# Optimization experiments

Measured on AMD Instinct MI355X. Metric: run time of the kernel, lower is better.

## Reference

```python
import math
import jax, jax.numpy as jnp
import numpy as np

B, S, D, H, FF, E, V, RH = 8, 256, 512, 8, 2048, 8, 32000, 256
MAX_PATH, MAX_VISITS = 4, 2
NEG = -1e9
DH = D // H


def _make_pe():
    # PositionalEncoding buffer (sin/cos), sliced to seq len S
    pos = np.arange(S, dtype=np.float32)[:, None]
    div = np.exp(np.arange(0, D, 2, dtype=np.float32) * (-math.log(10000.0) / D))
    pe = np.zeros((S, D), dtype=np.float32)
    pe[:, 0::2] = np.sin(pos * div)
    pe[:, 1::2] = np.cos(pos * div)
    return jnp.asarray(pe[None])  # [1,S,D]


def setup_inputs() -> dict:
    key = jax.random.key(0)
    ks = jax.random.split(key, 12)
    s = 0.02
    return dict(
        input_ids=jax.random.randint(ks[0], (B, S), 0, V),
        emb=jax.random.normal(ks[1], (V, D), jnp.float32) * s,
        pe=_make_pe(),
        Wqkv=jax.random.normal(ks[2], (E, 3 * D, D), jnp.float32) * s,
        bqkv=jnp.zeros((E, 3 * D), jnp.float32),
        Wo=jax.random.normal(ks[3], (E, D, D), jnp.float32) * s,
        bo=jnp.zeros((E, D), jnp.float32),
        W1=jax.random.normal(ks[4], (E, FF, D), jnp.float32) * s,
        b1=jnp.zeros((E, FF), jnp.float32),
        W2=jax.random.normal(ks[5], (E, D, FF), jnp.float32) * s,
        b2=jnp.zeros((E, D), jnp.float32),
        ln1_g=jnp.ones((E, D), jnp.float32), ln1_b=jnp.zeros((E, D), jnp.float32),
        ln2_g=jnp.ones((E, D), jnp.float32), ln2_b=jnp.zeros((E, D), jnp.float32),
        tag=jax.random.normal(ks[6], (E, D), jnp.float32) * 0.01,
        r_w1=jax.random.normal(ks[7], (RH, D), jnp.float32) * s,
        r_b1=jnp.zeros((RH,), jnp.float32),
        r_w2=jax.random.normal(ks[8], (E + 1, RH), jnp.float32) * s,
        r_b2=jnp.zeros((E + 1,), jnp.float32),
        lm_w=jax.random.normal(ks[9], (V, D), jnp.float32) * s,
        lm_b=jnp.zeros((V,), jnp.float32),
    )


def _ln(x, g, b):
    # per-sample gathered LayerNorm params g,b: [B,D]; x: [B,S,D]
    mu = x.mean(-1, keepdims=True)
    var = ((x - mu) ** 2).mean(-1, keepdims=True)
    return (x - mu) * jax.lax.rsqrt(var + 1e-5) * g[:, None, :] + b[:, None, :]


def _expert(x, idx, Wqkv, bqkv, Wo, bo, W1, b1, W2, b2, g1, be1, g2, be2, tag):
    # post-norm TransformerEncoderLayer (eval mode, dropout off) with per-sample expert params
    qkv = jnp.einsum('bsd,bfd->bsf', x, Wqkv[idx]) + bqkv[idx][:, None, :]
    q, k, v = jnp.split(qkv, 3, axis=-1)
    q = q.reshape(B, S, H, DH)
    k = k.reshape(B, S, H, DH)
    v = v.reshape(B, S, H, DH)
    att = jax.nn.softmax(jnp.einsum('bqhd,bkhd->bhqk', q, k) / math.sqrt(DH), axis=-1)
    ctx = jnp.einsum('bhqk,bkhd->bqhd', att, v).reshape(B, S, D)
    attn_out = jnp.einsum('bsd,bod->bso', ctx, Wo[idx]) + bo[idx][:, None, :]
    x = _ln(x + attn_out, g1[idx], be1[idx])
    hid = jax.nn.relu(jnp.einsum('bsd,bfd->bsf', x, W1[idx]) + b1[idx][:, None, :])
    ff = jnp.einsum('bsf,bdf->bsd', hid, W2[idx]) + b2[idx][:, None, :]
    x = _ln(x + ff, g2[idx], be2[idx])
    return x + tag[idx][:, None, :]  # + specialization_tag


def reference(input_ids, emb, pe, Wqkv, bqkv, Wo, bo, W1, b1, W2, b2,
              ln1_g, ln1_b, ln2_g, ln2_b, tag, r_w1, r_b1, r_w2, r_b2, lm_w, lm_b):
    pad_mask = (jnp.arange(V) != 0).astype(emb.dtype)[:, None]  # padding_idx=0 row is zero
    rep = (emb * pad_mask)[input_ids] * math.sqrt(D) + pe[:, :S]
    visits = jnp.zeros((B, E), jnp.int32)
    active = jnp.ones((B,), bool)
    ent_total = jnp.asarray(0.0, rep.dtype)
    for _ in range(MAX_PATH):
        summary = rep.mean(1)  # [B,D]
        h = jax.nn.relu(summary @ r_w1.T + r_b1)
        logits = h @ r_w2.T + r_b2  # [B,E+1], last slot = terminate
        logits = jnp.concatenate(
            [jnp.where(visits >= MAX_VISITS, NEG, logits[:, :E]), logits[:, E:]], axis=1)
        probs = jax.nn.softmax(logits, axis=-1)
        ent = -jnp.sum(probs * jnp.log(probs + 1e-9), axis=-1)
        cnt = jnp.sum(active)
        ent_total = ent_total + jnp.where(
            cnt > 0, jnp.sum(ent * active) / jnp.maximum(cnt, 1).astype(ent.dtype), 0.0)
        choice = jnp.argmax(logits, axis=-1)       # eval mode: hard argmax
        go = active & (choice < E)                 # samples routed to an expert this step
        idx = jnp.where(go, choice, 0)
        visits = visits + jax.nn.one_hot(idx, E, dtype=jnp.int32) * go[:, None].astype(jnp.int32)
        new_rep = _expert(rep, idx, Wqkv, bqkv, Wo, bo, W1, b1, W2, b2,
                          ln1_g, ln1_b, ln2_g, ln2_b, tag)
        rep = jnp.where(go[:, None, None], new_rep, rep)  # terminated/inactive reps frozen
        active = go
    logits_lm = rep @ lm_w.T + lm_b  # [B,S,V]
    return logits_lm, ent_total
```

## Files before the change

kernel.cpp:

```cpp
#include <hip/hip_runtime.h>
#include <hip/hip_bf16.h>

#define NB 8
#define NS 256
#define ND 512
#define NH 8
#define NDH 64
#define NFF 2048
#define NE 8
#define NV 32000
#define NRH 256
#define MAXV 2
#define NEGV (-1e9f)

typedef __attribute__((ext_vector_type(8))) short short8;
typedef __attribute__((ext_vector_type(4))) float f32x4;

__device__ __forceinline__ unsigned short f2bf(float x) {
  unsigned int u = __float_as_uint(x);
  u = (u + 0x7fffu + ((u >> 16) & 1u)) >> 16;
  return (unsigned short)u;
}

__device__ __forceinline__ void gload16(const unsigned short* g, unsigned short* l) {
  __builtin_amdgcn_global_load_lds(
      (const __attribute__((address_space(1))) unsigned int*)g,
      (__attribute__((address_space(3))) unsigned int*)l, 16, 0, 0);
}

__device__ __forceinline__ int swzc(int lane) {
  return (lane & 3) ^ ((lane >> 3) & 3);
}

__device__ __forceinline__ void cast8(const float* s, unsigned short* d, int j) {
  const float4* s4 = (const float4*)s;
  float4 a = s4[j * 2], b = s4[j * 2 + 1];
  short8 v;
  v[0] = (short)f2bf(a.x); v[1] = (short)f2bf(a.y);
  v[2] = (short)f2bf(a.z); v[3] = (short)f2bf(a.w);
  v[4] = (short)f2bf(b.x); v[5] = (short)f2bf(b.y);
  v[6] = (short)f2bf(b.z); v[7] = (short)f2bf(b.w);
  *(short8*)&d[(size_t)j * 8] = v;
}

__global__ __launch_bounds__(256) void k_cast5(
    const float* s0, unsigned short* d0, int n0,
    const float* s1, unsigned short* d1, int n1,
    const float* s2, unsigned short* d2, int n2,
    const float* s3, unsigned short* d3, int n3,
    const float* s4, unsigned short* d4, int n4,
    int* visits, int* active, float* entp) {
  if (blockIdx.x == 0) {
    if (threadIdx.x < NB * NE) visits[threadIdx.x] = 0;
    if (threadIdx.x < NB) active[threadIdx.x] = 1;
    if (threadIdx.x == 0) *entp = 0.f;
  }
  int j = blockIdx.x * 256 + threadIdx.x;
  if (j < n0) { cast8(s0, d0, j); return; }
  j -= n0;
  if (j < n1) { cast8(s1, d1, j); return; }
  j -= n1;
  if (j < n2) { cast8(s2, d2, j); return; }
  j -= n2;
  if (j < n3) { cast8(s3, d3, j); return; }
  j -= n3;
  if (j < n4) cast8(s4, d4, j);
}

__global__ __launch_bounds__(256) void k_embed16(const int* __restrict__ ids,
                                                 const float* __restrict__ emb,
                                                 const float* __restrict__ pe,
                                                 float* __restrict__ rep,
                                                 unsigned short* __restrict__ repb,
                                                 float* __restrict__ partial) {
  int rg = blockIdx.x, b = blockIdx.y;
  int t = threadIdx.x;
  int c0 = t, c1 = t + 256;
  float p0 = 0.f, p1 = 0.f;
  for (int row = 0; row < 16; ++row) {
    int s = rg * 16 + row;
    int id = ids[b * NS + s];
    float sc = (id != 0) ? 22.627416997969522f : 0.f;
    float v0 = emb[(size_t)id * ND + c0] * sc + pe[(size_t)s * ND + c0];
    float v1 = emb[(size_t)id * ND + c1] * sc + pe[(size_t)s * ND + c1];
    size_t base = ((size_t)b * NS + s) * ND;
    rep[base + c0] = v0; rep[base + c1] = v1;
    repb[base + c0] = f2bf(v0); repb[base + c1] = f2bf(v1);
    p0 += v0; p1 += v1;
  }
  float* pp = partial + ((size_t)b * 16 + rg) * ND;
  pp[c0] = p0; pp[c1] = p1;
}

__global__ __launch_bounds__(256) void k_router(const float* __restrict__ partial,
                                                const float* __restrict__ rw1,
                                                const float* __restrict__ rb1,
                                                const float* __restrict__ rw2,
                                                const float* __restrict__ rb2,
                                                int* visits, int* active,
                                                int* idx, int* go, float* ent_total) {
  __shared__ float sm[NB][ND];
  __shared__ float h[NB][NRH];
  __shared__ float lg[NB][NE + 1];
  int t = threadIdx.x;
  for (int i = t; i < NB * ND; i += 256) {
    int bb = i >> 9, d = i & 511;
    const float* pp = partial + ((size_t)bb * 16) * ND + d;
    float s = 0.f;
#pragma unroll
    for (int rg = 0; rg < 16; ++rg) s += pp[(size_t)rg * ND];
    sm[bb][d] = s * (1.f / NS);
  }
  __syncthreads();
  {
    const float* w = rw1 + (size_t)t * ND;
    float acc[NB];
#pragma unroll
    for (int b = 0; b < NB; ++b) acc[b] = rb1[t];
    for (int d = 0; d < ND; ++d) {
      float wv = w[d];
#pragma unroll
      for (int b = 0; b < NB; ++b) acc[b] += sm[b][d] * wv;
    }
#pragma unroll
    for (int b = 0; b < NB; ++b) h[b][t] = fmaxf(acc[b], 0.f);
  }
  __syncthreads();
  if (t < NB * (NE + 1)) {
    int b = t / (NE + 1), e = t % (NE + 1);
    const float* w = rw2 + e * NRH;
    float a = rb2[e];
    for (int r = 0; r < NRH; ++r) a += h[b][r] * w[r];
    lg[b][e] = a;
  }
  __syncthreads();
  if (t == 0) {
    int aprev[NB];
    int cnt = 0;
    for (int b = 0; b < NB; ++b) { aprev[b] = active[b]; cnt += aprev[b]; }
    float entsum = 0.f;
    for (int b = 0; b < NB; ++b) {
      float l[NE + 1];
      for (int e = 0; e < NE; ++e)
        l[e] = (visits[b * NE + e] >= MAXV) ? NEGV : lg[b][e];
      l[NE] = lg[b][NE];
      float m = l[0];
      for (int e = 1; e <= NE; ++e) m = fmaxf(m, l[e]);
      float z = 0.f, p[NE + 1];
      for (int e = 0; e <= NE; ++e) { p[e] = __expf(l[e] - m); z += p[e]; }
      float zi = 1.f / z, ent = 0.f;
      for (int e = 0; e <= NE; ++e) {
        float pp = p[e] * zi;
        ent -= pp * __logf(pp + 1e-9f);
      }
      if (aprev[b]) entsum += ent;
      int ch = 0; float bm = l[0];
      for (int e = 1; e <= NE; ++e) if (l[e] > bm) { bm = l[e]; ch = e; }
      int g = (aprev[b] && ch < NE) ? 1 : 0;
      int ix = g ? ch : 0;
      visits[b * NE + ix] += g;
      idx[b] = ix; go[b] = g; active[b] = g;
    }
    if (cnt > 0) *ent_total += entsum / (float)cnt;
  }
}

template <int OUT, int RELU>
__global__ __launch_bounds__(256) void k_gemm64(
    const unsigned short* __restrict__ Aall, int sa,
    const unsigned short* __restrict__ Wall, const float* __restrict__ ball,
    float* __restrict__ Fall, unsigned short* __restrict__ Uall, int so,
    int N, int K,
    unsigned short* __restrict__ Qb, unsigned short* __restrict__ Kb,
    unsigned short* __restrict__ Vt,
    const int* __restrict__ go, const int* __restrict__ idx) {
  int b = blockIdx.z;
  if (!go[b]) return;
  int t = threadIdx.x;
  int lane = t & 63, w = t >> 6;
  int wm = (w >> 1) * 32, wn = (w & 1) * 32;
  int bm = blockIdx.x * 64, bn = blockIdx.y * 64;
  int lrow = (lane >> 4) * 4, lcol = lane & 15;
  const unsigned short* A = Aall + (size_t)b * sa;
  const unsigned short* W = Wall + (size_t)idx[b] * N * K;
  const float* bias = ball + (size_t)idx[b] * N;

  __shared__ __align__(16) unsigned short As[2][64][32];
  __shared__ __align__(16) unsigned short Bs[2][64][32];
  f32x4 acc[2][2];
#pragma unroll
  for (int i = 0; i < 2; ++i)
#pragma unroll
    for (int j = 0; j < 2; ++j) acc[i][j] = (f32x4){0.f, 0.f, 0.f, 0.f};

  const unsigned short* ga = A + (size_t)(bm + w * 16 + (lane >> 2)) * K + swzc(lane) * 8;
  const unsigned short* gb = W + (size_t)(bn + w * 16 + (lane >> 2)) * K + swzc(lane) * 8;

  gload16(ga, &As[0][w * 16][0]);
  gload16(gb, &Bs[0][w * 16][0]);
  __syncthreads();

  int nk = K >> 5;
  int row0 = lane & 15;
  int cs = ((lane >> 4) ^ ((row0 >> 1) & 3)) * 8;
  for (int it = 0; it < nk; ++it) {
    int cur = it & 1;
    if (it + 1 < nk) {
      gload16(ga + (it + 1) * 32, &As[cur ^ 1][w * 16][0]);
      gload16(gb + (it + 1) * 32, &Bs[cur ^ 1][w * 16][0]);
    }
    short8 a[2], bfr[2];
#pragma unroll
    for (int mf = 0; mf < 2; ++mf)
      a[mf] = *(const short8*)&As[cur][wm + mf * 16 + row0][cs];
#pragma unroll
    for (int nf = 0; nf < 2; ++nf)
      bfr[nf] = *(const short8*)&Bs[cur][wn + nf * 16 + row0][cs];
#pragma unroll
    for (int mf = 0; mf < 2; ++mf)
#pragma unroll
      for (int nf = 0; nf < 2; ++nf)
        acc[mf][nf] = __builtin_amdgcn_mfma_f32_16x16x32_bf16(a[mf], bfr[nf], acc[mf][nf], 0, 0, 0);
    __syncthreads();
  }

  if (OUT == 2) {
    int seg = bn >> 9;
#pragma unroll
    for (int nf = 0; nf < 2; ++nf) {
      int col = bn + wn + nf * 16 + lcol;
      float bv = bias[col];
      if (seg < 2) {
        unsigned short* dst = (seg == 0) ? Qb : Kb;
        int cc = col - seg * 512;
#pragma unroll
        for (int mf = 0; mf < 2; ++mf)
#pragma unroll
          for (int r = 0; r < 4; ++r) {
            int row = bm + wm + mf * 16 + lrow + r;
            dst[((size_t)b * NS + row) * ND + cc] = f2bf(acc[mf][nf][r] + bv);
          }
      } else {
        int dcol = col - 1024;
#pragma unroll
        for (int mf = 0; mf < 2; ++mf) {
          int s0 = bm + wm + mf * 16 + lrow;
          unsigned long long pk =
              (unsigned long long)f2bf(acc[mf][nf][0] + bv) |
              ((unsigned long long)f2bf(acc[mf][nf][1] + bv) << 16) |
              ((unsigned long long)f2bf(acc[mf][nf][2] + bv) << 32) |
              ((unsigned long long)f2bf(acc[mf][nf][3] + bv) << 48);
          *(unsigned long long*)&Vt[((size_t)b * 512 + dcol) * 256 + s0] = pk;
        }
      }
    }
  } else {
#pragma unroll
    for (int nf = 0; nf < 2; ++nf) {
      int col = bn + wn + nf * 16 + lcol;
      float bv = bias[col];
#pragma unroll
      for (int mf = 0; mf < 2; ++mf) {
#pragma unroll
        for (int r = 0; r < 4; ++r) {
          int row = bm + wm + mf * 16 + lrow + r;
          float v = acc[mf][nf][r] + bv;
          if (RELU) v = fmaxf(v, 0.f);
          if (OUT == 0)
            Fall[(size_t)b * so + (size_t)row * N + col] = v;
          else
            Uall[(size_t)b * so + (size_t)row * N + col] = f2bf(v);
        }
      }
    }
  }
}

__global__ __launch_bounds__(256) void k_attn2(const unsigned short* __restrict__ Qb,
                                               const unsigned short* __restrict__ Kb,
                                               const unsigned short* __restrict__ Vt,
                                               unsigned short* __restrict__ ctxb,
                                               const int* __restrict__ go) {
  int b = blockIdx.z, h = blockIdx.y, qt = blockIdx.x;
  if (!go[b]) return;
  int t = threadIdx.x;
  __shared__ __align__(16) unsigned short lds0[16384];
  __shared__ __align__(16) unsigned short lds1[16384];
  int lane = t & 63, w = t >> 6, g = lane >> 4, c = lane & 15;

#pragma unroll
  for (int i = 0; i < 8; ++i) {
    int task = i * 256 + t;
    int k = task >> 3, cc = task & 7;
    short8 v = *(const short8*)&Kb[((size_t)b * NS + k) * ND + h * NDH + cc * 8];
    *(short8*)&lds0[k * 64 + ((cc * 8) ^ ((k & 7) << 3))] = v;
  }
#pragma unroll
  for (int i = 0; i < 8; ++i) {
    int task = i * 256 + t;
    int d = task >> 5, kc = task & 31;
    short8 v = *(const short8*)&Vt[((size_t)b * 512 + h * NDH + d) * 256 + kc * 8];
    *(short8*)&lds1[d * 256 + ((kc * 8) ^ ((d & 7) << 3))] = v;
  }
  short8 qf[2];
  {
    const unsigned short* qp = Qb + ((size_t)b * NS + qt * 64 + w * 16 + c) * ND + h * NDH;
    qf[0] = *(const short8*)&qp[g * 8];
    qf[1] = *(const short8*)&qp[32 + g * 8];
  }
  __syncthreads();

  f32x4 sacc[16];
#pragma unroll
  for (int mf = 0; mf < 16; ++mf) sacc[mf] = (f32x4){0.f, 0.f, 0.f, 0.f};
#pragma unroll
  for (int mf = 0; mf < 16; ++mf) {
#pragma unroll
    for (int kd = 0; kd < 2; ++kd) {
      int row = mf * 16 + c;
      short8 kf = *(const short8*)&lds0[row * 64 + ((kd * 32 + g * 8) ^ ((row & 7) << 3))];
      sacc[mf] = __builtin_amdgcn_mfma_f32_16x16x32_bf16(kf, qf[kd], sacc[mf], 0, 0, 0);
    }
  }
  __syncthreads();

  float mx = -3.4e38f;
#pragma unroll
  for (int mf = 0; mf < 16; ++mf) {
#pragma unroll
    for (int r = 0; r < 4; ++r) {
      sacc[mf][r] *= 0.125f;
      mx = fmaxf(mx, sacc[mf][r]);
    }
  }
  mx = fmaxf(mx, __shfl_xor(mx, 16));
  mx = fmaxf(mx, __shfl_xor(mx, 32));
  float sum = 0.f;
#pragma unroll
  for (int mf = 0; mf < 16; ++mf)
#pragma unroll
    for (int r = 0; r < 4; ++r) {
      float p = __expf(sacc[mf][r] - mx);
      sacc[mf][r] = p;
      sum += p;
    }
  sum += __shfl_xor(sum, 16);
  sum += __shfl_xor(sum, 32);
  float zi = 1.f / sum;

  int q_l = w * 16 + c;
#pragma unroll
  for (int mf = 0; mf < 16; ++mf) {
    unsigned long long pk =
        (unsigned long long)f2bf(sacc[mf][0] * zi) |
        ((unsigned long long)f2bf(sacc[mf][1] * zi) << 16) |
        ((unsigned long long)f2bf(sacc[mf][2] * zi) << 32) |
        ((unsigned long long)f2bf(sacc[mf][3] * zi) << 48);
    *(unsigned long long*)&lds0[q_l * 256 + ((mf * 16 + g * 4) ^ ((q_l & 7) << 3))] = pk;
  }

  f32x4 cacc[4];
#pragma unroll
  for (int nf = 0; nf < 4; ++nf) cacc[nf] = (f32x4){0.f, 0.f, 0.f, 0.f};
#pragma unroll
  for (int ks = 0; ks < 8; ++ks) {
    int prow = w * 16 + c;
    short8 pf = *(const short8*)&lds0[prow * 256 + ((ks * 32 + g * 8) ^ ((prow & 7) << 3))];
#pragma unroll
    for (int nf = 0; nf < 4; ++nf) {
      int vrow = nf * 16 + c;
      short8 vf = *(const short8*)&lds1[vrow * 256 + ((ks * 32 + g * 8) ^ ((vrow & 7) << 3))];
      cacc[nf] = __builtin_amdgcn_mfma_f32_16x16x32_bf16(pf, vf, cacc[nf], 0, 0, 0);
    }
  }
#pragma unroll
  for (int nf = 0; nf < 4; ++nf)
#pragma unroll
    for (int r = 0; r < 4; ++r)
      ctxb[((size_t)b * NS + qt * 64 + w * 16 + g * 4 + r) * ND + h * NDH + nf * 16 + c] =
          f2bf(cacc[nf][r]);
}

__global__ __launch_bounds__(256) void k_lnw(const float* __restrict__ xin,
                                             const float* __restrict__ yin,
                                             const float* __restrict__ gall,
                                             const float* __restrict__ ball,
                                             float* __restrict__ outf,
                                             unsigned short* __restrict__ outb,
                                             const int* __restrict__ go,
                                             const int* __restrict__ idx) {
  int b = blockIdx.y;
  if (!go[b]) return;
  int w = threadIdx.x >> 6, l = threadIdx.x & 63;
  int s = blockIdx.x * 4 + w;
  size_t base = ((size_t)b * NS + s) * ND;
  int d = l * 8;
  float4 x0 = *(const float4*)&xin[base + d];
  float4 x1 = *(const float4*)&xin[base + d + 4];
  float4 y0 = *(const float4*)&yin[base + d];
  float4 y1 = *(const float4*)&yin[base + d + 4];
  float v[8] = {x0.x + y0.x, x0.y + y0.y, x0.z + y0.z, x0.w + y0.w,
                x1.x + y1.x, x1.y + y1.y, x1.z + y1.z, x1.w + y1.w};
  float sum = 0.f;
#pragma unroll
  for (int j = 0; j < 8; ++j) sum += v[j];
#pragma unroll
  for (int off = 1; off < 64; off <<= 1) sum += __shfl_xor(sum, off);
  float mu = sum * (1.f / ND);
  float var = 0.f;
#pragma unroll
  for (int j = 0; j < 8; ++j) { v[j] -= mu; var += v[j] * v[j]; }
#pragma unroll
  for (int off = 1; off < 64; off <<= 1) var += __shfl_xor(var, off);
  float rs = rsqrtf(var * (1.f / ND) + 1e-5f);
  int ix = idx[b];
  float4 g0 = *(const float4*)&gall[ix * ND + d];
  float4 g1 = *(const float4*)&gall[ix * ND + d + 4];
  float4 b0 = *(const float4*)&ball[ix * ND + d];
  float4 b1 = *(const float4*)&ball[ix * ND + d + 4];
  float gg[8] = {g0.x, g0.y, g0.z, g0.w, g1.x, g1.y, g1.z, g1.w};
  float bb[8] = {b0.x, b0.y, b0.z, b0.w, b1.x, b1.y, b1.z, b1.w};
  float o[8];
#pragma unroll
  for (int j = 0; j < 8; ++j) o[j] = v[j] * rs * gg[j] + bb[j];
  *(float4*)&outf[base + d] = (float4){o[0], o[1], o[2], o[3]};
  *(float4*)&outf[base + d + 4] = (float4){o[4], o[5], o[6], o[7]};
  short8 ob;
#pragma unroll
  for (int j = 0; j < 8; ++j) ob[j] = (short)f2bf(o[j]);
  *(short8*)&outb[base + d] = ob;
}

__global__ __launch_bounds__(256) void k_lnw_p(const float* __restrict__ xin,
                                               const float* __restrict__ yin,
                                               const float* __restrict__ gall,
                                               const float* __restrict__ ball,
                                               const float* __restrict__ tagall,
                                               float* __restrict__ outf,
                                               unsigned short* __restrict__ outb,
                                               float* __restrict__ partial,
                                               const int* __restrict__ go,
                                               const int* __restrict__ idx) {
  int b = blockIdx.y;
  if (!go[b]) return;
  int rg = blockIdx.x;
  int w = threadIdx.x >> 6, l = threadIdx.x & 63;
  int ix = idx[b];
  int d = l * 8;
  float4 g0 = *(const float4*)&gall[ix * ND + d];
  float4 g1 = *(const float4*)&gall[ix * ND + d + 4];
  float4 b0 = *(const float4*)&ball[ix * ND + d];
  float4 b1 = *(const float4*)&ball[ix * ND + d + 4];
  float4 t0 = *(const float4*)&tagall[ix * ND + d];
  float4 t1 = *(const float4*)&tagall[ix * ND + d + 4];
  float gg[8] = {g0.x, g0.y, g0.z, g0.w, g1.x, g1.y, g1.z, g1.w};
  float bb[8] = {b0.x + t0.x, b0.y + t0.y, b0.z + t0.z, b0.w + t0.w,
                 b1.x + t1.x, b1.y + t1.y, b1.z + t1.z, b1.w + t1.w};
  float p[8] = {0.f, 0.f, 0.f, 0.f, 0.f, 0.f, 0.f, 0.f};
  for (int rr = 0; rr < 4; ++rr) {
    int s = rg * 16 + w * 4 + rr;
    size_t base = ((size_t)b * NS + s) * ND;
    float4 x0 = *(const float4*)&xin[base + d];
    float4 x1 = *(const float4*)&xin[base + d + 4];
    float4 y0 = *(const float4*)&yin[base + d];
    float4 y1 = *(const float4*)&yin[base + d + 4];
    float v[8] = {x0.x + y0.x, x0.y + y0.y, x0.z + y0.z, x0.w + y0.w,
                  x1.x + y1.x, x1.y + y1.y, x1.z + y1.z, x1.w + y1.w};
    float sum = 0.f;
#pragma unroll
    for (int j = 0; j < 8; ++j) sum += v[j];
#pragma unroll
    for (int off = 1; off < 64; off <<= 1) sum += __shfl_xor(sum, off);
    float mu = sum * (1.f / ND);
    float var = 0.f;
#pragma unroll
    for (int j = 0; j < 8; ++j) { v[j] -= mu; var += v[j] * v[j]; }
#pragma unroll
    for (int off = 1; off < 64; off <<= 1) var += __shfl_xor(var, off);
    float rs = rsqrtf(var * (1.f / ND) + 1e-5f);
    float o[8];
    short8 ob;
#pragma unroll
    for (int j = 0; j < 8; ++j) {
      o[j] = v[j] * rs * gg[j] + bb[j];
      p[j] += o[j];
      ob[j] = (short)f2bf(o[j]);
    }
    *(float4*)&outf[base + d] = (float4){o[0], o[1], o[2], o[3]};
    *(float4*)&outf[base + d + 4] = (float4){o[4], o[5], o[6], o[7]};
    *(short8*)&outb[base + d] = ob;
  }
  __shared__ float pl[4][ND];
#pragma unroll
  for (int j = 0; j < 8; ++j) pl[w][d + j] = p[j];
  __syncthreads();
  if (w == 0) {
    float* pp = partial + ((size_t)b * 16 + rg) * ND;
#pragma unroll
    for (int j = 0; j < 8; ++j)
      pp[d + j] = pl[0][d + j] + pl[1][d + j] + pl[2][d + j] + pl[3][d + j];
  }
}

__global__ __launch_bounds__(512, 2) void k_lmhead256(const unsigned short* __restrict__ Ab,
                                                      const unsigned short* __restrict__ Wb,
                                                      const float* __restrict__ bias,
                                                      float* __restrict__ out,
                                                      const float* __restrict__ entp) {
  if (blockIdx.x == 0 && threadIdx.x == 0)
    out[(size_t)NB * NS * NV] = *entp;
  int id = blockIdx.x;
  int swz = (id & 7) * 125 + (id >> 3);
  int bm = (swz % 8) * 256;
  int bn = (swz / 8) * 256;

  __shared__ __align__(16) unsigned short As[2][256][32];
  __shared__ __align__(16) unsigned short Bs[2][256][32];
  int t = threadIdx.x;
  int lane = t & 63, w = t >> 6;
  int wm = (w >> 2) * 128, wn = (w & 3) * 64;
  f32x4 acc[8][4];
#pragma unroll
  for (int i = 0; i < 8; ++i)
#pragma unroll
    for (int j = 0; j < 4; ++j) acc[i][j] = (f32x4){0.f, 0.f, 0.f, 0.f};

  const unsigned short* ga = Ab + (size_t)(bm + w * 32 + (lane >> 2)) * ND + swzc(lane) * 8;
  const unsigned short* gb = Wb + (size_t)(bn + w * 32 + (lane >> 2)) * ND + swzc(lane) * 8;

  gload16(ga, &As[0][w * 32][0]);
  gload16(ga + 16 * ND, &As[0][w * 32 + 16][0]);
  gload16(gb, &Bs[0][w * 32][0]);
  gload16(gb + 16 * ND, &Bs[0][w * 32 + 16][0]);
  __syncthreads();

  int row0 = lane & 15;
  int cs = ((lane >> 4) ^ ((row0 >> 1) & 3)) * 8;
  for (int it = 0; it < 16; ++it) {
    int cur = it & 1;
    if (it < 15) {
      int k0 = (it + 1) * 32;
      gload16(ga + k0, &As[cur ^ 1][w * 32][0]);
      gload16(ga + k0 + 16 * ND, &As[cur ^ 1][w * 32 + 16][0]);
      gload16(gb + k0, &Bs[cur ^ 1][w * 32][0]);
      gload16(gb + k0 + 16 * ND, &Bs[cur ^ 1][w * 32 + 16][0]);
    }
    short8 a[8], bfr[4];
#pragma unroll
    for (int mf = 0; mf < 8; ++mf)
      a[mf] = *(const short8*)&As[cur][wm + mf * 16 + row0][cs];
#pragma unroll
    for (int nf = 0; nf < 4; ++nf)
      bfr[nf] = *(const short8*)&Bs[cur][wn + nf * 16 + row0][cs];
#pragma unroll
    for (int mf = 0; mf < 8; ++mf)
#pragma unroll
      for (int nf = 0; nf < 4; ++nf)
        acc[mf][nf] = __builtin_amdgcn_mfma_f32_16x16x32_bf16(a[mf], bfr[nf], acc[mf][nf], 0, 0, 0);
    __syncthreads();
  }
  int lrow = (lane >> 4) * 4, lcol = lane & 15;
#pragma unroll
  for (int nf = 0; nf < 4; ++nf) {
    int col = bn + wn + nf * 16 + lcol;
    float bv = bias[col];
#pragma unroll
    for (int mf = 0; mf < 8; ++mf) {
#pragma unroll
      for (int r = 0; r < 4; ++r) {
        int row = bm + wm + mf * 16 + lrow + r;
        out[(size_t)row * NV + col] = acc[mf][nf][r] + bv;
      }
    }
  }
}

extern "C" void kernel_launch(void* const* d_in, const int* in_sizes, int n_in,
                              void* d_out, int out_size, void* d_ws, size_t ws_size,
                              hipStream_t stream) {
  const int* ids   = (const int*)d_in[0];
  const float* emb = (const float*)d_in[1];
  const float* pe  = (const float*)d_in[2];
  const float* Wqkv = (const float*)d_in[3];
  const float* bqkv = (const float*)d_in[4];
  const float* Wo   = (const float*)d_in[5];
  const float* bo   = (const float*)d_in[6];
  const float* W1   = (const float*)d_in[7];
  const float* b1   = (const float*)d_in[8];
  const float* W2   = (const float*)d_in[9];
  const float* b2   = (const float*)d_in[10];
  const float* g1   = (const float*)d_in[11];
  const float* be1  = (const float*)d_in[12];
  const float* g2   = (const float*)d_in[13];
  const float* be2  = (const float*)d_in[14];
  const float* tag  = (const float*)d_in[15];
  const float* rw1  = (const float*)d_in[16];
  const float* rb1  = (const float*)d_in[17];
  const float* rw2  = (const float*)d_in[18];
  const float* rb2  = (const float*)d_in[19];
  const float* lmw  = (const float*)d_in[20];
  const float* lmb  = (const float*)d_in[21];
  float* out = (float*)d_out;

  float* ws = (float*)d_ws;
  size_t o = 0;
  float* rep = ws + o;  o += (size_t)NB * NS * ND;
  float* x1  = ws + o;  o += (size_t)NB * NS * ND;
  float* tmp = ws + o;  o += (size_t)NB * NS * ND;
  float* partial = ws + o; o += (size_t)NB * 16 * ND;
  int* visits = (int*)(ws + o); o += 1024;
  int* active = visits + NB * NE;
  int* idx = active + NB;
  int* go = idx + NB;
  float* entp = (float*)(go + NB);

  unsigned short* us = (unsigned short*)(ws + o);
  size_t uo = 0;
  unsigned short* rep_b = us + uo; uo += (size_t)NB * NS * ND;
  unsigned short* x1_b  = us + uo; uo += (size_t)NB * NS * ND;
  unsigned short* ctx_b = us + uo; uo += (size_t)NB * NS * ND;
  unsigned short* Qb    = us + uo; uo += (size_t)NB * NS * ND;
  unsigned short* Kb    = us + uo; uo += (size_t)NB * NS * ND;
  unsigned short* Vt    = us + uo; uo += (size_t)NB * NS * ND;
  unsigned short* hid_b = us + uo; uo += (size_t)NB * NS * NFF;
  unsigned short* Wqkv_b = us + uo; uo += (size_t)NE * 3 * ND * ND;
  unsigned short* Wo_b   = us + uo; uo += (size_t)NE * ND * ND;
  unsigned short* W1_b   = us + uo; uo += (size_t)NE * NFF * ND;
  unsigned short* W2_b   = us + uo; uo += (size_t)NE * ND * NFF;
  unsigned short* lmw_b  = us + uo; uo += (size_t)NV * ND;

  {
    int n0 = NE * 3 * ND * ND / 8, n1 = NE * ND * ND / 8, n2 = NE * NFF * ND / 8,
        n3 = NE * ND * NFF / 8, n4 = NV * ND / 8;
    int nblk = (n0 + n1 + n2 + n3 + n4) / 256;
    k_cast5<<<nblk, 256, 0, stream>>>(Wqkv, Wqkv_b, n0, Wo, Wo_b, n1,
                                      W1, W1_b, n2, W2, W2_b, n3, lmw, lmw_b, n4,
                                      visits, active, entp);
  }

  k_embed16<<<dim3(16, NB), 256, 0, stream>>>(ids, emb, pe, rep, rep_b, partial);

  for (int step = 0; step < 4; ++step) {
    k_router<<<1, 256, 0, stream>>>(partial, rw1, rb1, rw2, rb2,
                                    visits, active, idx, go, entp);
    k_gemm64<2, 0><<<dim3(4, 24, NB), 256, 0, stream>>>(
        rep_b, NS * ND, Wqkv_b, bqkv, nullptr, nullptr, 0, 3 * ND, ND,
        Qb, Kb, Vt, go, idx);
    k_attn2<<<dim3(4, NH, NB), 256, 0, stream>>>(Qb, Kb, Vt, ctx_b, go);
    k_gemm64<0, 0><<<dim3(4, 8, NB), 256, 0, stream>>>(
        ctx_b, NS * ND, Wo_b, bo, tmp, nullptr, NS * ND, ND, ND,
        nullptr, nullptr, nullptr, go, idx);
    k_lnw<<<dim3(NS / 4, NB), 256, 0, stream>>>(rep, tmp, g1, be1,
                                                x1, x1_b, go, idx);
    k_gemm64<1, 1><<<dim3(4, 32, NB), 256, 0, stream>>>(
        x1_b, NS * ND, W1_b, b1, nullptr, hid_b, NS * NFF, NFF, ND,
        nullptr, nullptr, nullptr, go, idx);
    k_gemm64<0, 0><<<dim3(4, 8, NB), 256, 0, stream>>>(
        hid_b, NS * NFF, W2_b, b2, tmp, nullptr, NS * ND, ND, NFF,
        nullptr, nullptr, nullptr, go, idx);
    k_lnw_p<<<dim3(16, NB), 256, 0, stream>>>(x1, tmp, g2, be2, tag,
                                              rep, rep_b, partial, go, idx);
  }

  k_lmhead256<<<1000, 512, 0, stream>>>(rep_b, lmw_b, lmb, out, entp);
}
```

Before: 626.6 us.

## Split-K the narrow GEMMs, widen N tiles, fold embed into the cast kernel

The Wo and W2 projections (N=512) now use split-K across 2 and 4 chunks, writing fp32 partials. The following LayerNorm kernel sums those partials and adds the bias, which raises parallelism on the low-block-count GEMMs. The QKV and W1 GEMMs switch to 64x128 tiles so more B data is reused per block. The embedding kernel is merged into the weight-cast launch to save one launch. The cost is extra partial-buffer traffic (up to 4 fp32 copies of the activations) and more registers per thread in the wider tiles.

```diff
diff --git a/kernel.cpp b/kernel.cpp
--- a/kernel.cpp
+++ b/kernel.cpp
@@ -43,17 +43,42 @@
   *(short8*)&d[(size_t)j * 8] = v;
 }
 
-__global__ __launch_bounds__(256) void k_cast5(
+__global__ __launch_bounds__(256) void k_cast5e(
     const float* s0, unsigned short* d0, int n0,
     const float* s1, unsigned short* d1, int n1,
     const float* s2, unsigned short* d2, int n2,
     const float* s3, unsigned short* d3, int n3,
     const float* s4, unsigned short* d4, int n4,
+    int nbcast,
+    const int* __restrict__ ids, const float* __restrict__ emb,
+    const float* __restrict__ pe, float* __restrict__ rep,
+    unsigned short* __restrict__ repb, float* __restrict__ partial,
     int* visits, int* active, float* entp) {
   if (blockIdx.x == 0) {
     if (threadIdx.x < NB * NE) visits[threadIdx.x] = 0;
     if (threadIdx.x < NB) active[threadIdx.x] = 1;
     if (threadIdx.x == 0) *entp = 0.f;
+  }
+  if ((int)blockIdx.x >= nbcast) {
+    int j2 = blockIdx.x - nbcast;
+    int rg = j2 & 15, b = j2 >> 4;
+    int t = threadIdx.x;
+    int c0 = t, c1 = t + 256;
+    float p0 = 0.f, p1 = 0.f;
+    for (int row = 0; row < 16; ++row) {
+      int s = rg * 16 + row;
+      int id = ids[b * NS + s];
+      float sc = (id != 0) ? 22.627416997969522f : 0.f;
+      float v0 = emb[(size_t)id * ND + c0] * sc + pe[(size_t)s * ND + c0];
+      float v1 = emb[(size_t)id * ND + c1] * sc + pe[(size_t)s * ND + c1];
+      size_t base = ((size_t)b * NS + s) * ND;
+      rep[base + c0] = v0; rep[base + c1] = v1;
+      repb[base + c0] = f2bf(v0); repb[base + c1] = f2bf(v1);
+      p0 += v0; p1 += v1;
+    }
+    float* pp = partial + ((size_t)b * 16 + rg) * ND;
+    pp[c0] = p0; pp[c1] = p1;
+    return;
   }
   int j = blockIdx.x * 256 + threadIdx.x;
   if (j < n0) { cast8(s0, d0, j); return; }
@@ -65,31 +90,6 @@
   if (j < n3) { cast8(s3, d3, j); return; }
   j -= n3;
   if (j < n4) cast8(s4, d4, j);
-}
-
-__global__ __launch_bounds__(256) void k_embed16(const int* __restrict__ ids,
-                                                 const float* __restrict__ emb,
-                                                 const float* __restrict__ pe,
-                                                 float* __restrict__ rep,
-                                                 unsigned short* __restrict__ repb,
-                                                 float* __restrict__ partial) {
-  int rg = blockIdx.x, b = blockIdx.y;
-  int t = threadIdx.x;
-  int c0 = t, c1 = t + 256;
-  float p0 = 0.f, p1 = 0.f;
-  for (int row = 0; row < 16; ++row) {
-    int s = rg * 16 + row;
-    int id = ids[b * NS + s];
-    float sc = (id != 0) ? 22.627416997969522f : 0.f;
-    float v0 = emb[(size_t)id * ND + c0] * sc + pe[(size_t)s * ND + c0];
-    float v1 = emb[(size_t)id * ND + c1] * sc + pe[(size_t)s * ND + c1];
-    size_t base = ((size_t)b * NS + s) * ND;
-    rep[base + c0] = v0; rep[base + c1] = v1;
-    repb[base + c0] = f2bf(v0); repb[base + c1] = f2bf(v1);
-    p0 += v0; p1 += v1;
-  }
-  float* pp = partial + ((size_t)b * 16 + rg) * ND;
-  pp[c0] = p0; pp[c1] = p1;
 }
 
 __global__ __launch_bounds__(256) void k_router(const float* __restrict__ partial,
@@ -166,11 +166,10 @@
 }
 
 template <int OUT, int RELU>
-__global__ __launch_bounds__(256) void k_gemm64(
+__global__ __launch_bounds__(256) void k_gemmN128(
     const unsigned short* __restrict__ Aall, int sa,
     const unsigned short* __restrict__ Wall, const float* __restrict__ ball,
-    float* __restrict__ Fall, unsigned short* __restrict__ Uall, int so,
-    int N, int K,
+    unsigned short* __restrict__ Uall, int so, int N, int K,
     unsigned short* __restrict__ Qb, unsigned short* __restrict__ Kb,
     unsigned short* __restrict__ Vt,
     const int* __restrict__ go, const int* __restrict__ idx) {
@@ -178,26 +177,27 @@
   if (!go[b]) return;
   int t = threadIdx.x;
   int lane = t & 63, w = t >> 6;
-  int wm = (w >> 1) * 32, wn = (w & 1) * 32;
-  int bm = blockIdx.x * 64, bn = blockIdx.y * 64;
+  int wm = (w >> 1) * 32, wn = (w & 1) * 64;
+  int bm = blockIdx.x * 64, bn = blockIdx.y * 128;
   int lrow = (lane >> 4) * 4, lcol = lane & 15;
   const unsigned short* A = Aall + (size_t)b * sa;
   const unsigned short* W = Wall + (size_t)idx[b] * N * K;
   const float* bias = ball + (size_t)idx[b] * N;
 
   __shared__ __align__(16) unsigned short As[2][64][32];
-  __shared__ __align__(16) unsigned short Bs[2][64][32];
-  f32x4 acc[2][2];
+  __shared__ __align__(16) unsigned short Bs[2][128][32];
+  f32x4 acc[2][4];
 #pragma unroll
   for (int i = 0; i < 2; ++i)
 #pragma unroll
-    for (int j = 0; j < 2; ++j) acc[i][j] = (f32x4){0.f, 0.f, 0.f, 0.f};
+    for (int j = 0; j < 4; ++j) acc[i][j] = (f32x4){0.f, 0.f, 0.f, 0.f};
 
   const unsigned short* ga = A + (size_t)(bm + w * 16 + (lane >> 2)) * K + swzc(lane) * 8;
-  const unsigned short* gb = W + (size_t)(bn + w * 16 + (lane >> 2)) * K + swzc(lane) * 8;
+  const unsigned short* gb = W + (size_t)(bn + w * 32 + (lane >> 2)) * K + swzc(lane) * 8;
 
   gload16(ga, &As[0][w * 16][0]);
-  gload16(gb, &Bs[0][w * 16][0]);
+  gload16(gb, &Bs[0][w * 32][0]);
+  gload16(gb + 16 * (size_t)K, &Bs[0][w * 32 + 16][0]);
   __syncthreads();
 
   int nk = K >> 5;
@@ -207,19 +207,20 @@
     int cur = it & 1;
     if (it + 1 < nk) {
       gload16(ga + (it + 1) * 32, &As[cur ^ 1][w * 16][0]);
-      gload16(gb + (it + 1) * 32, &Bs[cur ^ 1][w * 16][0]);
-    }
-    short8 a[2], bfr[2];
+      gload16(gb + (it + 1) * 32, &Bs[cur ^ 1][w * 32][0]);
+      gload16(gb + (it + 1) * 32 + 16 * (size_t)K, &Bs[cur ^ 1][w * 32 + 16][0]);
+    }
+    short8 a[2], bfr[4];
 #pragma unroll
     for (int mf = 0; mf < 2; ++mf)
       a[mf] = *(const short8*)&As[cur][wm + mf * 16 + row0][cs];
 #pragma unroll
-    for (int nf = 0; nf < 2; ++nf)
+    for (int nf = 0; nf < 4; ++nf)
       bfr[nf] = *(const short8*)&Bs[cur][wn + nf * 16 + row0][cs];
 #pragma unroll
     for (int mf = 0; mf < 2; ++mf)
 #pragma unroll
-      for (int nf = 0; nf < 2; ++nf)
+      for (int nf = 0; nf < 4; ++nf)
         acc[mf][nf] = __builtin_amdgcn_mfma_f32_16x16x32_bf16(a[mf], bfr[nf], acc[mf][nf], 0, 0, 0);
     __syncthreads();
   }
@@ -227,7 +228,7 @@
   if (OUT == 2) {
     int seg = bn >> 9;
 #pragma unroll
-    for (int nf = 0; nf < 2; ++nf) {
+    for (int nf = 0; nf < 4; ++nf) {
       int col = bn + wn + nf * 16 + lcol;
       float bv = bias[col];
       if (seg < 2) {
@@ -256,7 +257,7 @@
     }
   } else {
 #pragma unroll
-    for (int nf = 0; nf < 2; ++nf) {
+    for (int nf = 0; nf < 4; ++nf) {
       int col = bn + wn + nf * 16 + lcol;
       float bv = bias[col];
 #pragma unroll
@@ -266,13 +267,79 @@
           int row = bm + wm + mf * 16 + lrow + r;
           float v = acc[mf][nf][r] + bv;
           if (RELU) v = fmaxf(v, 0.f);
-          if (OUT == 0)
-            Fall[(size_t)b * so + (size_t)row * N + col] = v;
-          else
-            Uall[(size_t)b * so + (size_t)row * N + col] = f2bf(v);
+          Uall[(size_t)b * so + (size_t)row * N + col] = f2bf(v);
         }
       }
     }
+  }
+}
+
+template <int NCH>
+__global__ __launch_bounds__(256) void k_gemm64sk(
+    const unsigned short* __restrict__ Aall, int sa,
+    const unsigned short* __restrict__ Wall,
+    float* __restrict__ Pall, int N, int K,
+    const int* __restrict__ go, const int* __restrict__ idx) {
+  int b = blockIdx.z;
+  if (!go[b]) return;
+  int t = threadIdx.x;
+  int lane = t & 63, w = t >> 6;
+  int wm = (w >> 1) * 32, wn = (w & 1) * 32;
+  int kc = blockIdx.x >> 2;
+  int bm = (blockIdx.x & 3) * 64, bn = blockIdx.y * 64;
+  int KC = K / NCH;
+  int lrow = (lane >> 4) * 4, lcol = lane & 15;
+  const unsigned short* A = Aall + (size_t)b * sa + kc * KC;
+  const unsigned short* W = Wall + (size_t)idx[b] * N * K + kc * KC;
+
+  __shared__ __align__(16) unsigned short As[2][64][32];
+  __shared__ __align__(16) unsigned short Bs[2][64][32];
+  f32x4 acc[2][2];
+#pragma unroll
+  for (int i = 0; i < 2; ++i)
+#pragma unroll
+    for (int j = 0; j < 2; ++j) acc[i][j] = (f32x4){0.f, 0.f, 0.f, 0.f};
+
+  const unsigned short* ga = A + (size_t)(bm + w * 16 + (lane >> 2)) * K + swzc(lane) * 8;
+  const unsigned short* gb = W + (size_t)(bn + w * 16 + (lane >> 2)) * K + swzc(lane) * 8;
+
+  gload16(ga, &As[0][w * 16][0]);
+  gload16(gb, &Bs[0][w * 16][0]);
+  __syncthreads();
+
+  int nk = KC >> 5;
+  int row0 = lane & 15;
+  int cs = ((lane >> 4) ^ ((row0 >> 1) & 3)) * 8;
+  for (int it = 0; it < nk; ++it) {
+    int cur = it & 1;
+    if (it + 1 < nk) {
+      gload16(ga + (it + 1) * 32, &As[cur ^ 1][w * 16][0]);
+      gload16(gb + (it + 1) * 32, &Bs[cur ^ 1][w * 16][0]);
+    }
+    short8 a[2], bfr[2];
+#pragma unroll
+    for (int mf = 0; mf < 2; ++mf)
+      a[mf] = *(const short8*)&As[cur][wm + mf * 16 + row0][cs];
+#pragma unroll
+    for (int nf = 0; nf < 2; ++nf)
+      bfr[nf] = *(const short8*)&Bs[cur][wn + nf * 16 + row0][cs];
+#pragma unroll
+    for (int mf = 0; mf < 2; ++mf)
+#pragma unroll
+      for (int nf = 0; nf < 2; ++nf)
+        acc[mf][nf] = __builtin_amdgcn_mfma_f32_16x16x32_bf16(a[mf], bfr[nf], acc[mf][nf], 0, 0, 0);
+    __syncthreads();
+  }
+
+  float* P = Pall + ((size_t)kc * NB + b) * ((size_t)NS * N);
+#pragma unroll
+  for (int nf = 0; nf < 2; ++nf) {
+    int col = bn + wn + nf * 16 + lcol;
+#pragma unroll
+    for (int mf = 0; mf < 2; ++mf)
+#pragma unroll
+      for (int r = 0; r < 4; ++r)
+        P[(size_t)(bm + wm + mf * 16 + lrow + r) * N + col] = acc[mf][nf][r];
   }
 }
 
@@ -381,91 +448,59 @@
           f2bf(cacc[nf][r]);
 }
 
-__global__ __launch_bounds__(256) void k_lnw(const float* __restrict__ xin,
-                                             const float* __restrict__ yin,
-                                             const float* __restrict__ gall,
-                                             const float* __restrict__ ball,
-                                             float* __restrict__ outf,
-                                             unsigned short* __restrict__ outb,
-                                             const int* __restrict__ go,
-                                             const int* __restrict__ idx) {
-  int b = blockIdx.y;
-  if (!go[b]) return;
-  int w = threadIdx.x >> 6, l = threadIdx.x & 63;
-  int s = blockIdx.x * 4 + w;
-  size_t base = ((size_t)b * NS + s) * ND;
-  int d = l * 8;
-  float4 x0 = *(const float4*)&xin[base + d];
-  float4 x1 = *(const float4*)&xin[base + d + 4];
-  float4 y0 = *(const float4*)&yin[base + d];
-  float4 y1 = *(const float4*)&yin[base + d + 4];
-  float v[8] = {x0.x + y0.x, x0.y + y0.y, x0.z + y0.z, x0.w + y0.w,
-                x1.x + y1.x, x1.y + y1.y, x1.z + y1.z, x1.w + y1.w};
-  float sum = 0.f;
-#pragma unroll
-  for (int j = 0; j < 8; ++j) sum += v[j];
-#pragma unroll
-  for (int off = 1; off < 64; off <<= 1) sum += __shfl_xor(sum, off);
-  float mu = sum * (1.f / ND);
-  float var = 0.f;
-#pragma unroll
-  for (int j = 0; j < 8; ++j) { v[j] -= mu; var += v[j] * v[j]; }
-#pragma unroll
-  for (int off = 1; off < 64; off <<= 1) var += __shfl_xor(var, off);
-  float rs = rsqrtf(var * (1.f / ND) + 1e-5f);
-  int ix = idx[b];
-  float4 g0 = *(const float4*)&gall[ix * ND + d];
-  float4 g1 = *(const float4*)&gall[ix * ND + d + 4];
-  float4 b0 = *(const float4*)&ball[ix * ND + d];
-  float4 b1 = *(const float4*)&ball[ix * ND + d + 4];
-  float gg[8] = {g0.x, g0.y, g0.z, g0.w, g1.x, g1.y, g1.z, g1.w};
-  float bb[8] = {b0.x, b0.y, b0.z, b0.w, b1.x, b1.y, b1.z, b1.w};
-  float o[8];
-#pragma unroll
-  for (int j = 0; j < 8; ++j) o[j] = v[j] * rs * gg[j] + bb[j];
-  *(float4*)&outf[base + d] = (float4){o[0], o[1], o[2], o[3]};
-  *(float4*)&outf[base + d + 4] = (float4){o[4], o[5], o[6], o[7]};
-  short8 ob;
-#pragma unroll
-  for (int j = 0; j < 8; ++j) ob[j] = (short)f2bf(o[j]);
-  *(short8*)&outb[base + d] = ob;
-}
-
-__global__ __launch_bounds__(256) void k_lnw_p(const float* __restrict__ xin,
-                                               const float* __restrict__ yin,
-                                               const float* __restrict__ gall,
-                                               const float* __restrict__ ball,
-                                               const float* __restrict__ tagall,
-                                               float* __restrict__ outf,
-                                               unsigned short* __restrict__ outb,
-                                               float* __restrict__ partial,
-                                               const int* __restrict__ go,
-                                               const int* __restrict__ idx) {
+template <int NCH, int TAG, int SUMP>
+__global__ __launch_bounds__(256) void k_ln_red(
+    const float* __restrict__ res, const float* __restrict__ part,
+    const float* __restrict__ gbias,
+    const float* __restrict__ gall, const float* __restrict__ beall,
+    const float* __restrict__ tagall,
+    float* __restrict__ outf, unsigned short* __restrict__ outb,
+    float* __restrict__ sump,
+    const int* __restrict__ go, const int* __restrict__ idx) {
   int b = blockIdx.y;
   if (!go[b]) return;
   int rg = blockIdx.x;
   int w = threadIdx.x >> 6, l = threadIdx.x & 63;
   int ix = idx[b];
   int d = l * 8;
-  float4 g0 = *(const float4*)&gall[ix * ND + d];
-  float4 g1 = *(const float4*)&gall[ix * ND + d + 4];
-  float4 b0 = *(const float4*)&ball[ix * ND + d];
-  float4 b1 = *(const float4*)&ball[ix * ND + d + 4];
-  float4 t0 = *(const float4*)&tagall[ix * ND + d];
-  float4 t1 = *(const float4*)&tagall[ix * ND + d + 4];
-  float gg[8] = {g0.x, g0.y, g0.z, g0.w, g1.x, g1.y, g1.z, g1.w};
-  float bb[8] = {b0.x + t0.x, b0.y + t0.y, b0.z + t0.z, b0.w + t0.w,
-                 b1.x + t1.x, b1.y + t1.y, b1.z + t1.z, b1.w + t1.w};
-  float p[8] = {0.f, 0.f, 0.f, 0.f, 0.f, 0.f, 0.f, 0.f};
+  float gb8[8], gg[8], bb[8];
+  {
+    float4 a0 = *(const float4*)&gbias[ix * ND + d];
+    float4 a1 = *(const float4*)&gbias[ix * ND + d + 4];
+    gb8[0] = a0.x; gb8[1] = a0.y; gb8[2] = a0.z; gb8[3] = a0.w;
+    gb8[4] = a1.x; gb8[5] = a1.y; gb8[6] = a1.z; gb8[7] = a1.w;
+    float4 g0 = *(const float4*)&gall[ix * ND + d];
+    float4 g1 = *(const float4*)&gall[ix * ND + d + 4];
+    gg[0] = g0.x; gg[1] = g0.y; gg[2] = g0.z; gg[3] = g0.w;
+    gg[4] = g1.x; gg[5] = g1.y; gg[6] = g1.z; gg[7] = g1.w;
+    float4 b0 = *(const float4*)&beall[ix * ND + d];
+    float4 b1 = *(const float4*)&beall[ix * ND + d + 4];
+    bb[0] = b0.x; bb[1] = b0.y; bb[2] = b0.z; bb[3] = b0.w;
+    bb[4] = b1.x; bb[5] = b1.y; bb[6] = b1.z; bb[7] = b1.w;
+    if (TAG) {
+      float4 t0 = *(const float4*)&tagall[ix * ND + d];
+      float4 t1 = *(const float4*)&tagall[ix * ND + d + 4];
+      bb[0] += t0.x; bb[1] += t0.y; bb[2] += t0.z; bb[3] += t0.w;
+      bb[4] += t1.x; bb[5] += t1.y; bb[6] += t1.z; bb[7] += t1.w;
+    }
+  }
+  float ps[8] = {0.f, 0.f, 0.f, 0.f, 0.f, 0.f, 0.f, 0.f};
+  const size_t CSTRIDE = (size_t)NB * NS * ND;
   for (int rr = 0; rr < 4; ++rr) {
     int s = rg * 16 + w * 4 + rr;
     size_t base = ((size_t)b * NS + s) * ND;
-    float4 x0 = *(const float4*)&xin[base + d];
-    float4 x1 = *(const float4*)&xin[base + d + 4];
-    float4 y0 = *(const float4*)&yin[base + d];
-    float4 y1 = *(const float4*)&yin[base + d + 4];
-    float v[8] = {x0.x + y0.x, x0.y + y0.y, x0.z + y0.z, x0.w + y0.w,
-                  x1.x + y1.x, x1.y + y1.y, x1.z + y1.z, x1.w + y1.w};
+    float4 x0 = *(const float4*)&res[base + d];
+    float4 x1 = *(const float4*)&res[base + d + 4];
+    float v[8] = {x0.x + gb8[0], x0.y + gb8[1], x0.z + gb8[2], x0.w + gb8[3],
+                  x1.x + gb8[4], x1.y + gb8[5], x1.z + gb8[6], x1.w + gb8[7]};
+#pragma unroll
+    for (int c = 0; c < NCH; ++c) {
+      const float* pc = part + c * CSTRIDE + base;
+      float4 p0 = *(const float4*)&pc[d];
+      float4 p1 = *(const float4*)&pc[d + 4];
+      v[0] += p0.x; v[1] += p0.y; v[2] += p0.z; v[3] += p0.w;
+      v[4] += p1.x; v[5] += p1.y; v[6] += p1.z; v[7] += p1.w;
+    }
     float sum = 0.f;
 #pragma unroll
     for (int j = 0; j < 8; ++j) sum += v[j];
@@ -483,22 +518,24 @@
 #pragma unroll
     for (int j = 0; j < 8; ++j) {
       o[j] = v[j] * rs * gg[j] + bb[j];
-      p[j] += o[j];
+      if (SUMP) ps[j] += o[j];
       ob[j] = (short)f2bf(o[j]);
     }
     *(float4*)&outf[base + d] = (float4){o[0], o[1], o[2], o[3]};
     *(float4*)&outf[base + d + 4] = (float4){o[4], o[5], o[6], o[7]};
     *(short8*)&outb[base + d] = ob;
   }
-  __shared__ float pl[4][ND];
-#pragma unroll
-  for (int j = 0; j < 8; ++j) pl[w][d + j] = p[j];
-  __syncthreads();
-  if (w == 0) {
-    float* pp = partial + ((size_t)b * 16 + rg) * ND;
-#pragma unroll
-    for (int j = 0; j < 8; ++j)
-      pp[d + j] = pl[0][d + j] + pl[1][d + j] + pl[2][d + j] + pl[3][d + j];
+  if (SUMP) {
+    __shared__ float pl[4][ND];
+#pragma unroll
+    for (int j = 0; j < 8; ++j) pl[w][d + j] = ps[j];
+    __syncthreads();
+    if (w == 0) {
+      float* pp = sump + ((size_t)b * 16 + rg) * ND;
+#pragma unroll
+      for (int j = 0; j < 8; ++j)
+        pp[d + j] = pl[0][d + j] + pl[1][d + j] + pl[2][d + j] + pl[3][d + j];
+    }
   }
 }
 
@@ -606,7 +643,7 @@
   size_t o = 0;
   float* rep = ws + o;  o += (size_t)NB * NS * ND;
   float* x1  = ws + o;  o += (size_t)NB * NS * ND;
-  float* tmp = ws + o;  o += (size_t)NB * NS * ND;
+  float* partk = ws + o; o += (size_t)4 * NB * NS * ND;
   float* partial = ws + o; o += (size_t)NB * 16 * ND;
   int* visits = (int*)(ws + o); o += 1024;
   int* active = visits + NB * NE;
@@ -632,34 +669,30 @@
   {
     int n0 = NE * 3 * ND * ND / 8, n1 = NE * ND * ND / 8, n2 = NE * NFF * ND / 8,
         n3 = NE * ND * NFF / 8, n4 = NV * ND / 8;
-    int nblk = (n0 + n1 + n2 + n3 + n4) / 256;
-    k_cast5<<<nblk, 256, 0, stream>>>(Wqkv, Wqkv_b, n0, Wo, Wo_b, n1,
-                                      W1, W1_b, n2, W2, W2_b, n3, lmw, lmw_b, n4,
-                                      visits, active, entp);
-  }
-
-  k_embed16<<<dim3(16, NB), 256, 0, stream>>>(ids, emb, pe, rep, rep_b, partial);
+    int nbcast = (n0 + n1 + n2 + n3 + n4) / 256;
+    k_cast5e<<<nbcast + 16 * NB, 256, 0, stream>>>(
+        Wqkv, Wqkv_b, n0, Wo, Wo_b, n1, W1, W1_b, n2, W2, W2_b, n3, lmw, lmw_b, n4,
+        nbcast, ids, emb, pe, rep, rep_b, partial, visits, active, entp);
+  }
 
   for (int step = 0; step < 4; ++step) {
     k_router<<<1, 256, 0, stream>>>(partial, rw1, rb1, rw2, rb2,
                                     visits, active, idx, go, entp);
-    k_gemm64<2, 0><<<dim3(4, 24, NB), 256, 0, stream>>>(
-        rep_b, NS * ND, Wqkv_b, bqkv, nullptr, nullptr, 0, 3 * ND, ND,
+    k_gemmN128<2, 0><<<dim3(4, 12, NB), 256, 0, stream>>>(
+        rep_b, NS * ND, Wqkv_b, bqkv, nullptr, 0, 3 * ND, ND,
         Qb, Kb, Vt, go, idx);
     k_attn2<<<dim3(4, NH, NB), 256, 0, stream>>>(Qb, Kb, Vt, ctx_b, go);
-    k_gemm64<0, 0><<<dim3(4, 8, NB), 256, 0, stream>>>(
-        ctx_b, NS * ND, Wo_b, bo, tmp, nullptr, NS * ND, ND, ND,
+    k_gemm64sk<2><<<dim3(8, 8, NB), 256, 0, stream>>>(
+        ctx_b, NS * ND, Wo_b, partk, ND, ND, go, idx);
+    k_ln_red<2, 0, 0><<<dim3(16, NB), 256, 0, stream>>>(
+        rep, partk, bo, g1, be1, nullptr, x1, x1_b, nullptr, go, idx);
+    k_gemmN128<1, 1><<<dim3(4, 16, NB), 256, 0, stream>>>(
+        x1_b, NS * ND, W1_b, b1, hid_b, NS * NFF, NFF, ND,
         nullptr, nullptr, nullptr, go, idx);
-    k_lnw<<<dim3(NS / 4, NB), 256, 0, stream>>>(rep, tmp, g1, be1,
-                                                x1, x1_b, go, idx);
-    k_gemm64<1, 1><<<dim3(4, 32, NB), 256, 0, stream>>>(
-        x1_b, NS * ND, W1_b, b1, nullptr, hid_b, NS * NFF, NFF, ND,
-        nullptr, nullptr, nullptr, go, idx);
-    k_gemm64<0, 0><<<dim3(4, 8, NB), 256, 0, stream>>>(
-        hid_b, NS * NFF, W2_b, b2, tmp, nullptr, NS * ND, ND, NFF,
-        nullptr, nullptr, nullptr, go, idx);
-    k_lnw_p<<<dim3(16, NB), 256, 0, stream>>>(x1, tmp, g2, be2, tag,
-                                              rep, rep_b, partial, go, idx);
+    k_gemm64sk<4><<<dim3(16, 8, NB), 256, 0, stream>>>(
+        hid_b, NS * NFF, W2_b, partk, ND, NFF, go, idx);
+    k_ln_red<4, 1, 1><<<dim3(16, NB), 256, 0, stream>>>(
+        x1, partk, b2, g2, be2, tag, rep, rep_b, partial, go, idx);
   }
 
   k_lmhead256<<<1000, 512, 0, stream>>>(rep_b, lmw_b, lmb, out, entp);
```

Measured after the change: 602.9 us. 3.8% less time.
